# Optimization experiments

Measured on AMD Instinct MI355X. Metric: run time of the kernel, lower is better.

## Reference

```python
import jax, jax.numpy as jnp
import numpy as np

EMBED_DIM = 512
NUM_HEADS = 8
HEAD_DIM = EMBED_DIM // NUM_HEADS
SCALE = 1.0 / HEAD_DIM ** 0.5


def setup_inputs() -> dict:
    key = jax.random.key(0)
    ks = jax.random.split(key, 7)
    B, C, H, W = 8, EMBED_DIM, 32, 32
    x = jax.random.normal(ks[0], (B, C, H, W), dtype=jnp.float32)
    s = 1.0 / np.sqrt(EMBED_DIM)
    return {
        "x": x,
        "ln_gamma": jnp.ones((EMBED_DIM,), jnp.float32),
        "ln_beta": jnp.zeros((EMBED_DIM,), jnp.float32),
        "w_qkv": jax.random.uniform(ks[1], (EMBED_DIM, 3 * EMBED_DIM), jnp.float32, -s, s),
        "b_qkv": jax.random.uniform(ks[2], (3 * EMBED_DIM,), jnp.float32, -s, s),
        "w_proj": jax.random.uniform(ks[3], (EMBED_DIM, EMBED_DIM), jnp.float32, -s, s),
        "b_proj": jax.random.uniform(ks[4], (EMBED_DIM,), jnp.float32, -s, s),
    }


def reference(x, ln_gamma, ln_beta, w_qkv, b_qkv, w_proj, b_proj):
    B, C, H, W = x.shape
    N = H * W
    # LayerNorm over channel dim (applied in NHWC layout in the original)
    xs = x.reshape(B, C, N).transpose(0, 2, 1)  # [B, N, C]
    mu = jnp.mean(xs, axis=-1, keepdims=True)
    var = jnp.mean(jnp.square(xs - mu), axis=-1, keepdims=True)
    xn = (xs - mu) / jnp.sqrt(var + 1e-5) * ln_gamma + ln_beta
    # QKV projection
    qkv = xn @ w_qkv + b_qkv                        # [B, N, 3C]
    qkv = qkv.reshape(B, N, 3, NUM_HEADS, HEAD_DIM)
    q = qkv[:, :, 0].transpose(0, 2, 1, 3)         # [B, h, N, d]
    k = qkv[:, :, 1].transpose(0, 2, 1, 3)
    v = qkv[:, :, 2].transpose(0, 2, 1, 3)
    # Scaled dot-product attention (full N x N scores, as in source)
    attn = jnp.einsum('bhnd,bhmd->bhnm', q, k) * SCALE
    attn = jax.nn.softmax(attn, axis=-1)
    o = jnp.einsum('bhnm,bhmd->bhnd', attn, v)     # [B, h, N, d]
    o = o.transpose(0, 2, 1, 3).reshape(B, N, C)
    # Output projection (dropout is identity in eval)
    o = o @ w_proj + b_proj
    return o.transpose(0, 2, 1).reshape(B, C, H, W)
```

## Files before the change

kernel.cpp:

```cpp
#include <hip/hip_runtime.h>
#include <hip/hip_bf16.h>
#include <math.h>

#define B_   8
#define C_   512
#define NH_  8
#define HD_  64
#define NSP  1024
#define M_   (B_*NSP)
#define NQKV 1536
#define SCALE_ 0.125f
#define S2L_  0.18033688f

typedef __attribute__((ext_vector_type(8))) __bf16 bf16x8;
typedef __attribute__((ext_vector_type(4))) float  f32x4;

__device__ __forceinline__ unsigned short f2bf(float f) {
  unsigned int u = __float_as_uint(f);
  u = u + 0x7fffu + ((u >> 16) & 1u);
  return (unsigned short)(u >> 16);
}

__device__ __forceinline__ unsigned int pk2bf(float a, float b) {
  __hip_bfloat162 t = __float22bfloat162_rn(make_float2(a, b));
  unsigned int u; __builtin_memcpy(&u, &t, 4);
  return u;
}

__device__ __forceinline__ void async16(const unsigned short* g, unsigned short* l) {
  __builtin_amdgcn_global_load_lds(
      (const __attribute__((address_space(1))) void*)g,
      (__attribute__((address_space(3))) void*)l, 16, 0, 0);
}

__global__ void ln_stats_kernel(const float* __restrict__ x,
                                float* __restrict__ psum,
                                float* __restrict__ psum2) {
  int tx = threadIdx.x & 31, ty = threadIdx.x >> 5;
  int cg  = blockIdx.x & 3;
  int nch = (blockIdx.x >> 2) & 31;
  int b   = blockIdx.x >> 7;
  int n0 = nch * 32;
  const float* xp = x + (size_t)b * C_ * NSP + n0 + tx;
  float s = 0.f, s2 = 0.f;
  for (int c = cg * 128 + ty; c < cg * 128 + 128; c += 8) {
    float v = xp[(size_t)c * NSP];
    s += v; s2 += v * v;
  }
  __shared__ float sh_s[8][32], sh_s2[8][32];
  sh_s[ty][tx] = s; sh_s2[ty][tx] = s2;
  __syncthreads();
  if (ty == 0) {
    float S = 0.f, S2 = 0.f;
    for (int j = 0; j < 8; j++) { S += sh_s[j][tx]; S2 += sh_s2[j][tx]; }
    psum [cg * M_ + b * NSP + n0 + tx] = S;
    psum2[cg * M_ + b * NSP + n0 + tx] = S2;
  }
}

__global__ __launch_bounds__(256) void applyw_kernel(
    const float* __restrict__ x, const float* __restrict__ psum,
    const float* __restrict__ psum2, const float* __restrict__ gamma,
    const float* __restrict__ beta, const float* __restrict__ wqkv,
    const float* __restrict__ wproj, unsigned short* __restrict__ xn,
    unsigned short* __restrict__ wqkvT, unsigned short* __restrict__ wprojT) {
  int tid = threadIdx.x;
  __shared__ float tile[64][65];
  int tx = tid & 63, ty = tid >> 6;
  if (blockIdx.x >= 1024) {
    const float* W; unsigned short* WT; int NW, t;
    if (blockIdx.x < 1216) { W = wqkv;  WT = wqkvT;  NW = NQKV; t = blockIdx.x - 1024; }
    else                   { W = wproj; WT = wprojT; NW = C_;   t = blockIdx.x - 1216; }
    int ntiles = NW >> 6;
    int kt = t / ntiles, nt = t - kt * ntiles;
    for (int i = ty; i < 64; i += 4)
      tile[i][tx] = W[(size_t)(kt * 64 + i) * NW + nt * 64 + tx];
    __syncthreads();
    for (int i = ty; i < 64; i += 4)
      WT[(size_t)(nt * 64 + i) * C_ + kt * 64 + tx] = f2bf(tile[tx][i]);
    return;
  }
  __shared__ float smu[64], srs[64];
  int c0 = (blockIdx.x & 7) * 64;
  int n0 = ((blockIdx.x >> 3) & 15) * 64;
  int b  = blockIdx.x >> 7;
  if (tid < 64) {
    int n = b * NSP + n0 + tid;
    float s  = psum [n] + psum [M_ + n] + psum [2 * M_ + n] + psum [3 * M_ + n];
    float s2 = psum2[n] + psum2[M_ + n] + psum2[2 * M_ + n] + psum2[3 * M_ + n];
    float mu = s * (1.0f / C_);
    float var = s2 * (1.0f / C_) - mu * mu;
    smu[tid] = mu;
    srs[tid] = rsqrtf(var + 1e-5f);
  }
  const float* xp = x + ((size_t)b * C_ + c0) * NSP + n0;
  for (int i = ty; i < 64; i += 4)
    tile[i][tx] = xp[(size_t)i * NSP + tx];
  __syncthreads();
  float g = gamma[c0 + tx], be = beta[c0 + tx];
  unsigned short* op = xn + ((size_t)(b * NSP + n0)) * C_ + c0 + tx;
  for (int i = ty; i < 64; i += 4) {
    float v = (tile[tx][i] - smu[i]) * srs[i] * g + be;
    op[(size_t)i * C_] = f2bf(v);
  }
}

__global__ __launch_bounds__(256) void gemm_qkv_kernel(
    const unsigned short* __restrict__ A,
    const unsigned short* __restrict__ Bt,
    const float* __restrict__ bias,
    unsigned short* __restrict__ out0, unsigned short* __restrict__ out1) {
  __shared__ __align__(16) char smem[24576];
  int tid = threadIdx.x;
  int wave = tid >> 6, lane = tid & 63, quad = lane >> 4, l15 = lane & 15;
  int n0 = blockIdx.x * 128, m0 = blockIdx.y * 64;
  int wm = (wave >> 1) * 32, wn = (wave & 1) * 64;
  int srow = lane >> 2, schunk = (lane & 3) * 8;
  auto stage = [&](int k0, int buf) {
    unsigned short* As = (unsigned short*)(smem + buf * 12288);
    unsigned short* Bs = (unsigned short*)(smem + buf * 12288 + 4096);
    async16(A + (size_t)(m0 + wave * 16 + srow) * 512 + k0 + schunk,
            As + wave * 16 * 32 + lane * 8);
#pragma unroll
    for (int j = 0; j < 2; j++) {
      int r0 = (wave + 4 * j) * 16;
      async16(Bt + (size_t)(n0 + r0 + srow) * 512 + k0 + schunk, Bs + r0 * 32 + lane * 8);
    }
  };
  f32x4 acc[2][4] = {};
  stage(0, 0);
  for (int kt = 0; kt < 16; kt++) {
    int cur = kt & 1;
    __syncthreads();
    if (kt < 15) stage((kt + 1) * 32, cur ^ 1);
    unsigned short* As = (unsigned short*)(smem + cur * 12288);
    unsigned short* Bs = (unsigned short*)(smem + cur * 12288 + 4096);
    bf16x8 a[2], bb[4];
#pragma unroll
    for (int mt = 0; mt < 2; mt++)
      a[mt] = *(const bf16x8*)(As + (wm + mt * 16 + l15) * 32 + quad * 8);
#pragma unroll
    for (int nt = 0; nt < 4; nt++)
      bb[nt] = *(const bf16x8*)(Bs + (wn + nt * 16 + l15) * 32 + quad * 8);
#pragma unroll
    for (int mt = 0; mt < 2; mt++)
#pragma unroll
      for (int nt = 0; nt < 4; nt++)
        acc[mt][nt] = __builtin_amdgcn_mfma_f32_16x16x32_bf16(
            a[mt], bb[nt], acc[mt][nt], 0, 0, 0);
  }
  if (n0 < 1024) {
    float sc = ((n0 + wn) < 512) ? S2L_ : 1.0f;
#pragma unroll
    for (int mt = 0; mt < 2; mt++)
#pragma unroll
      for (int nt = 0; nt < 4; nt++)
#pragma unroll
        for (int r = 0; r < 4; r++) {
          int row = m0 + wm + mt * 16 + quad * 4 + r;
          int col = n0 + wn + nt * 16 + l15;
          out0[(size_t)row * 1024 + col] = f2bf((acc[mt][nt][r] + bias[col]) * sc);
        }
  } else {
    __syncthreads();
    unsigned short* buf = (unsigned short*)smem + wave * (32 * 17);
    int b = m0 >> 10, nbase = m0 & 1023;
    for (int nc = 0; nc < 4; nc++) {
#pragma unroll
      for (int mt = 0; mt < 2; mt++)
#pragma unroll
        for (int r = 0; r < 4; r++) {
          int col = n0 + wn + nc * 16 + l15;
          buf[(mt * 16 + quad * 4 + r) * 17 + l15] = f2bf(acc[mt][nc][r] + bias[col]);
        }
      int ml = lane & 31;
#pragma unroll
      for (int j = 0; j < 8; j++) {
        int cl = j * 2 + (lane >> 5);
        int crel = n0 - 1024 + wn + nc * 16 + cl;
        out1[((size_t)b * C_ + crel) * NSP + nbase + wm + ml] = buf[ml * 17 + cl];
      }
    }
  }
}

__global__ __launch_bounds__(256) void gemm_proj_kernel(
    const unsigned short* __restrict__ A,
    const unsigned short* __restrict__ Bt,
    const float* __restrict__ bias,
    float* __restrict__ O) {
  __shared__ __align__(16) char smem[20480];
  int tid = threadIdx.x;
  int wave = tid >> 6, lane = tid & 63, quad = lane >> 4, l15 = lane & 15;
  int n0 = blockIdx.x * 128, m0 = blockIdx.y * 32;
  int wm = (wave >> 1) * 16, wn = (wave & 1) * 64;
  int srow = lane >> 2, schunk = (lane & 3) * 8;
  auto stage = [&](int k0, int buf) {
    unsigned short* As = (unsigned short*)(smem + buf * 10240);
    unsigned short* Bs = (unsigned short*)(smem + buf * 10240 + 2048);
    if (wave < 2)
      async16(A + (size_t)(m0 + wave * 16 + srow) * 512 + k0 + schunk,
              As + wave * 16 * 32 + lane * 8);
#pragma unroll
    for (int j = 0; j < 2; j++) {
      int r0 = (wave + 4 * j) * 16;
      async16(Bt + (size_t)(n0 + r0 + srow) * 512 + k0 + schunk, Bs + r0 * 32 + lane * 8);
    }
  };
  f32x4 acc[4] = {};
  stage(0, 0);
  for (int kt = 0; kt < 16; kt++) {
    int cur = kt & 1;
    __syncthreads();
    if (kt < 15) stage((kt + 1) * 32, cur ^ 1);
    unsigned short* As = (unsigned short*)(smem + cur * 10240);
    unsigned short* Bs = (unsigned short*)(smem + cur * 10240 + 2048);
    bf16x8 a, bb[4];
    a = *(const bf16x8*)(As + (wm + l15) * 32 + quad * 8);
#pragma unroll
    for (int nt = 0; nt < 4; nt++)
      bb[nt] = *(const bf16x8*)(Bs + (wn + nt * 16 + l15) * 32 + quad * 8);
#pragma unroll
    for (int nt = 0; nt < 4; nt++)
      acc[nt] = __builtin_amdgcn_mfma_f32_16x16x32_bf16(a, bb[nt], acc[nt], 0, 0, 0);
  }
  __syncthreads();
  float* buf = (float*)smem + wave * (16 * 17);
  int b = m0 >> 10, nbase = m0 & 1023;
  int ml = lane & 15, cg = lane >> 4;
  for (int nc = 0; nc < 4; nc++) {
#pragma unroll
    for (int r = 0; r < 4; r++) {
      int col = n0 + wn + nc * 16 + l15;
      buf[(quad * 4 + r) * 17 + l15] = acc[nc][r] + bias[col];
    }
#pragma unroll
    for (int j = 0; j < 4; j++) {
      int cl = j * 4 + cg;
      int c = n0 + wn + nc * 16 + cl;
      O[((size_t)b * C_ + c) * NSP + nbase + wm + ml] = buf[ml * 17 + cl];
    }
  }
}

__global__ __launch_bounds__(256, 3) void attn_kernel(
    const unsigned short* __restrict__ qk,
    const unsigned short* __restrict__ vt,
    unsigned short* __restrict__ o_ws) {
  __shared__ __align__(16) unsigned short Ks[2][64][64];
  __shared__ __align__(16) unsigned short Vts[2][64][64];
  __shared__ __align__(16) unsigned short Ps[4][32][68];
  int tid = threadIdx.x;
  int wave = tid >> 6, lane = tid & 63, quad = lane >> 4, l15 = lane & 15;
  int qw = wave & 1, kh = wave >> 1;
  int b = blockIdx.x >> 3, h = blockIdx.x & 7;
  int q0 = blockIdx.y * 64 + qw * 32;
  int srow = lane >> 3, scc = lane & 7, swz = scc ^ srow;
  uint4 ones4 = (l15 == 0) ? make_uint4(0x3F803F80u, 0x3F803F80u, 0x3F803F80u, 0x3F803F80u)
                           : make_uint4(0u, 0u, 0u, 0u);
  bf16x8 av5; __builtin_memcpy(&av5, &ones4, 16);
  bf16x8 bq[2][2];
#pragma unroll
  for (int mt = 0; mt < 2; mt++)
#pragma unroll
    for (int ks = 0; ks < 2; ks++)
      bq[mt][ks] = *(const bf16x8*)(
          qk + (size_t)(b * NSP + q0 + mt * 16 + l15) * 1024 +
          h * 64 + ks * 32 + quad * 8);
  f32x4 ot[4][2] = {};
  f32x4 lacc[2] = {};
  for (int it = 0; it < 8; it++) {
    int k0 = kh * 512 + it * 64;
    __syncthreads();
#pragma unroll
    for (int g = 0; g < 4; g++) {
      int row = qw * 32 + g * 8;
      async16(qk + (size_t)(b * NSP + k0 + row + srow) * 1024 + 512 + h * 64 + swz * 8,
              &Ks[kh][row][0]);
      async16(vt + ((size_t)(b * C_ + h * 64 + row + srow)) * NSP + k0 + swz * 8,
              &Vts[kh][row][0]);
    }
    __syncthreads();
    bf16x8 ak[4][2];
#pragma unroll
    for (int n4 = 0; n4 < 4; n4++)
#pragma unroll
      for (int ks = 0; ks < 2; ks++)
        ak[n4][ks] = *(const bf16x8*)(
            &Ks[kh][n4 * 16 + l15][((ks * 4 + quad) ^ (l15 & 7)) * 8]);
    f32x4 s[4][2] = {};
#pragma unroll
    for (int n4 = 0; n4 < 4; n4++)
#pragma unroll
      for (int mt = 0; mt < 2; mt++)
#pragma unroll
        for (int ks = 0; ks < 2; ks++)
          s[n4][mt] = __builtin_amdgcn_mfma_f32_16x16x32_bf16(
              ak[n4][ks], bq[mt][ks], s[n4][mt], 0, 0, 0);
#pragma unroll
    for (int mt = 0; mt < 2; mt++)
#pragma unroll
      for (int n4 = 0; n4 < 4; n4++) {
        float p0 = __builtin_amdgcn_exp2f(s[n4][mt][0]);
        float p1 = __builtin_amdgcn_exp2f(s[n4][mt][1]);
        float p2 = __builtin_amdgcn_exp2f(s[n4][mt][2]);
        float p3 = __builtin_amdgcn_exp2f(s[n4][mt][3]);
        *(uint2*)(&Ps[wave][mt * 16 + l15][n4 * 16 + quad * 4]) =
            make_uint2(pk2bf(p0, p1), pk2bf(p2, p3));
      }
    bf16x8 av[4][2], bp[2][2];
#pragma unroll
    for (int dt = 0; dt < 4; dt++)
#pragma unroll
      for (int ks = 0; ks < 2; ks++)
        av[dt][ks] = *(const bf16x8*)(
            &Vts[kh][dt * 16 + l15][((ks * 4 + quad) ^ (l15 & 7)) * 8]);
#pragma unroll
    for (int mt = 0; mt < 2; mt++)
#pragma unroll
      for (int ks = 0; ks < 2; ks++)
        bp[mt][ks] = *(const bf16x8*)(&Ps[wave][mt * 16 + l15][ks * 32 + quad * 8]);
#pragma unroll
    for (int dt = 0; dt < 4; dt++)
#pragma unroll
      for (int mt = 0; mt < 2; mt++)
#pragma unroll
        for (int ks = 0; ks < 2; ks++)
          ot[dt][mt] = __builtin_amdgcn_mfma_f32_16x16x32_bf16(
              av[dt][ks], bp[mt][ks], ot[dt][mt], 0, 0, 0);
#pragma unroll
    for (int mt = 0; mt < 2; mt++)
#pragma unroll
      for (int ks = 0; ks < 2; ks++)
        lacc[mt] = __builtin_amdgcn_mfma_f32_16x16x32_bf16(
            av5, bp[mt][ks], lacc[mt], 0, 0, 0);
  }
  float* Cb = (float*)&Ks[0][0][0];
  float* Lb = (float*)&Vts[0][0][0];
#pragma unroll
  for (int mt = 0; mt < 2; mt++) {
    __syncthreads();
    if (kh == 1) {
#pragma unroll
      for (int dt = 0; dt < 4; dt++)
        *(f32x4*)&Cb[(qw * 16 + l15) * 68 + dt * 16 + quad * 4] = ot[dt][mt];
      if (quad == 0) Lb[qw * 16 + l15] = lacc[mt][0];
    }
    __syncthreads();
    if (kh == 0) {
#pragma unroll
      for (int dt = 0; dt < 4; dt++)
        ot[dt][mt] += *(const f32x4*)&Cb[(qw * 16 + l15) * 68 + dt * 16 + quad * 4];
      float lsum = lacc[mt][0] + Lb[qw * 16 + l15];
      float lv = __shfl(lsum, l15);
      float inv = 1.f / lv;
      size_t rowoff = (size_t)(b * NSP + q0 + mt * 16 + l15) * 512 + h * 64;
#pragma unroll
      for (int dt = 0; dt < 4; dt++)
        *(uint2*)(o_ws + rowoff + dt * 16 + quad * 4) =
            make_uint2(pk2bf(ot[dt][mt][0] * inv, ot[dt][mt][1] * inv),
                       pk2bf(ot[dt][mt][2] * inv, ot[dt][mt][3] * inv));
    }
  }
}

extern "C" void kernel_launch(void* const* d_in, const int* in_sizes, int n_in,
                              void* d_out, int out_size, void* d_ws, size_t ws_size,
                              hipStream_t stream) {
  const float* x     = (const float*)d_in[0];
  const float* gamma = (const float*)d_in[1];
  const float* beta  = (const float*)d_in[2];
  const float* wqkv  = (const float*)d_in[3];
  const float* bqkv  = (const float*)d_in[4];
  const float* wproj = (const float*)d_in[5];
  const float* bproj = (const float*)d_in[6];
  char* ws = (char*)d_ws;
  float*          psum   = (float*)ws;
  float*          psum2  = (float*)(ws + 131072);
  unsigned short* wqkvT  = (unsigned short*)(ws + 262144);
  unsigned short* wprojT = (unsigned short*)(ws + 1835008);
  unsigned short* qk_bf  = (unsigned short*)(ws + 2359296);
  unsigned short* vt_bf  = (unsigned short*)(ws + 19136512);
  unsigned short* xn_bf  = (unsigned short*)(ws + 27525120);
  unsigned short* o_bf   = xn_bf;
  float* out = (float*)d_out;

  ln_stats_kernel<<<1024, 256, 0, stream>>>(x, psum, psum2);
  applyw_kernel<<<1024 + 192 + 64, 256, 0, stream>>>(x, psum, psum2, gamma, beta,
                                                     wqkv, wproj, xn_bf, wqkvT, wprojT);
  gemm_qkv_kernel<<<dim3(NQKV / 128, M_ / 64), 256, 0, stream>>>(
      xn_bf, wqkvT, bqkv, qk_bf, vt_bf);
  attn_kernel<<<dim3(B_ * NH_, NSP / 64), 256, 0, stream>>>(qk_bf, vt_bf, o_bf);
  gemm_proj_kernel<<<dim3(C_ / 128, M_ / 32), 256, 0, stream>>>(
      o_bf, wprojT, bproj, out);
}
```

Measured before the change: 158.8 us.

## Load K and V fragments directly from global memory, drop LDS staging and barriers

The attention kernel no longer stages K and V tiles into shared memory through async copies with two barriers per iteration. Each wave now reads its MFMA operand fragments straight from global memory, relying on L1/L2 to absorb reuse between the two query waves. This removes the per-iteration block syncs and frees LDS, which could allow higher occupancy. In exchange it duplicates global loads across waves and exposes global latency directly inside the MFMA loop, with no explicit prefetch.

```diff
diff --git a/kernel.cpp b/kernel.cpp
--- a/kernel.cpp
+++ b/kernel.cpp
@@ -247,15 +247,14 @@
     const unsigned short* __restrict__ qk,
     const unsigned short* __restrict__ vt,
     unsigned short* __restrict__ o_ws) {
-  __shared__ __align__(16) unsigned short Ks[2][64][64];
-  __shared__ __align__(16) unsigned short Vts[2][64][64];
   __shared__ __align__(16) unsigned short Ps[4][32][68];
+  __shared__ __align__(16) float Cb[2][16][68];
+  __shared__ float Lb[2][16];
   int tid = threadIdx.x;
   int wave = tid >> 6, lane = tid & 63, quad = lane >> 4, l15 = lane & 15;
   int qw = wave & 1, kh = wave >> 1;
   int b = blockIdx.x >> 3, h = blockIdx.x & 7;
   int q0 = blockIdx.y * 64 + qw * 32;
-  int srow = lane >> 3, scc = lane & 7, swz = scc ^ srow;
   uint4 ones4 = (l15 == 0) ? make_uint4(0x3F803F80u, 0x3F803F80u, 0x3F803F80u, 0x3F803F80u)
                            : make_uint4(0u, 0u, 0u, 0u);
   bf16x8 av5; __builtin_memcpy(&av5, &ones4, 16);
@@ -267,27 +266,21 @@
       bq[mt][ks] = *(const bf16x8*)(
           qk + (size_t)(b * NSP + q0 + mt * 16 + l15) * 1024 +
           h * 64 + ks * 32 + quad * 8);
+  const unsigned short* kbase =
+      qk + (size_t)b * NSP * 1024 + 512 + h * 64 + quad * 8;
+  const unsigned short* vbase =
+      vt + ((size_t)(b * C_ + h * 64 + l15)) * NSP + quad * 8;
   f32x4 ot[4][2] = {};
   f32x4 lacc[2] = {};
   for (int it = 0; it < 8; it++) {
     int k0 = kh * 512 + it * 64;
-    __syncthreads();
-#pragma unroll
-    for (int g = 0; g < 4; g++) {
-      int row = qw * 32 + g * 8;
-      async16(qk + (size_t)(b * NSP + k0 + row + srow) * 1024 + 512 + h * 64 + swz * 8,
-              &Ks[kh][row][0]);
-      async16(vt + ((size_t)(b * C_ + h * 64 + row + srow)) * NSP + k0 + swz * 8,
-              &Vts[kh][row][0]);
-    }
-    __syncthreads();
     bf16x8 ak[4][2];
 #pragma unroll
     for (int n4 = 0; n4 < 4; n4++)
 #pragma unroll
       for (int ks = 0; ks < 2; ks++)
         ak[n4][ks] = *(const bf16x8*)(
-            &Ks[kh][n4 * 16 + l15][((ks * 4 + quad) ^ (l15 & 7)) * 8]);
+            kbase + (size_t)(k0 + n4 * 16 + l15) * 1024 + ks * 32);
     f32x4 s[4][2] = {};
 #pragma unroll
     for (int n4 = 0; n4 < 4; n4++)
@@ -314,7 +307,7 @@
 #pragma unroll
       for (int ks = 0; ks < 2; ks++)
         av[dt][ks] = *(const bf16x8*)(
-            &Vts[kh][dt * 16 + l15][((ks * 4 + quad) ^ (l15 & 7)) * 8]);
+            vbase + (size_t)(dt * 16) * NSP + k0 + ks * 32);
 #pragma unroll
     for (int mt = 0; mt < 2; mt++)
 #pragma unroll
@@ -335,23 +328,21 @@
         lacc[mt] = __builtin_amdgcn_mfma_f32_16x16x32_bf16(
             av5, bp[mt][ks], lacc[mt], 0, 0, 0);
   }
-  float* Cb = (float*)&Ks[0][0][0];
-  float* Lb = (float*)&Vts[0][0][0];
 #pragma unroll
   for (int mt = 0; mt < 2; mt++) {
     __syncthreads();
     if (kh == 1) {
 #pragma unroll
       for (int dt = 0; dt < 4; dt++)
-        *(f32x4*)&Cb[(qw * 16 + l15) * 68 + dt * 16 + quad * 4] = ot[dt][mt];
-      if (quad == 0) Lb[qw * 16 + l15] = lacc[mt][0];
+        *(f32x4*)&Cb[qw][l15][dt * 16 + quad * 4] = ot[dt][mt];
+      if (quad == 0) Lb[qw][l15] = lacc[mt][0];
     }
     __syncthreads();
     if (kh == 0) {
 #pragma unroll
       for (int dt = 0; dt < 4; dt++)
-        ot[dt][mt] += *(const f32x4*)&Cb[(qw * 16 + l15) * 68 + dt * 16 + quad * 4];
-      float lsum = lacc[mt][0] + Lb[qw * 16 + l15];
+        ot[dt][mt] += *(const f32x4*)&Cb[qw][l15][dt * 16 + quad * 4];
+      float lsum = lacc[mt][0] + Lb[qw][l15];
       float lv = __shfl(lsum, l15);
       float inv = 1.f / lv;
       size_t rowoff = (size_t)(b * NSP + q0 + mt * 16 + l15) * 512 + h * 64;
```

Result: slower. 189.9 us (+19.6%).
